# Kernel tuning notes

Measured on AMD Instinct MI355X. Metric: run time of the kernel, lower is better.

The kernel has to match this reference:

```python
import jax, jax.numpy as jnp
import numpy as np

NODE_DIM = 128
N_NODES = 100000
N_EDGES = 600000


def setup_inputs() -> dict:
    key = jax.random.key(0)
    k_x, k_e, k_w1, k_b1, k_w2, k_b2 = jax.random.split(key, 6)
    x = jax.random.normal(k_x, (N_NODES, NODE_DIM), dtype=jnp.float32)
    edge_index = jax.random.randint(k_e, (2, N_EDGES), 0, N_NODES, dtype=jnp.int64)
    # nn.Linear default init: U(-1/sqrt(fan_in), 1/sqrt(fan_in))
    lim1 = 1.0 / np.sqrt(2 * NODE_DIM)
    W1 = jax.random.uniform(k_w1, (2 * NODE_DIM, NODE_DIM), minval=-lim1, maxval=lim1, dtype=jnp.float32)
    b1 = jax.random.uniform(k_b1, (NODE_DIM,), minval=-lim1, maxval=lim1, dtype=jnp.float32)
    lim2 = 1.0 / np.sqrt(NODE_DIM)
    W2 = jax.random.uniform(k_w2, (NODE_DIM, 1), minval=-lim2, maxval=lim2, dtype=jnp.float32)
    b2 = jax.random.uniform(k_b2, (1,), minval=-lim2, maxval=lim2, dtype=jnp.float32)
    return {"x": x, "edge_index": edge_index, "W1": W1, "b1": b1, "W2": W2, "b2": b2}


def reference(x, edge_index, W1, b1, W2, b2):
    src = edge_index[0]
    dst = edge_index[1]
    # [E, 2*node_dim] gathered pair features
    pair = jnp.concatenate([x[src], x[dst]], axis=-1)
    h = jax.nn.relu(pair @ W1 + b1)          # [E, node_dim]
    s = jax.nn.sigmoid(h @ W2 + b2)          # [E, 1]
    return s.squeeze(-1)                      # [E]
```

## Files before the change

kernel.cpp:

```cpp
#include <hip/hip_runtime.h>
#include <hip/hip_bf16.h>
#include <stdint.h>

#define NODE_DIM 128
#define N_NODES  100000
#define N_EDGES  600000
#define NOUT     256

#define QSTEP_INV 64.0f
#define QSTEP     (1.0f / 64.0f)

typedef __bf16 bf16x8 __attribute__((ext_vector_type(8)));
typedef float  f32x4  __attribute__((ext_vector_type(4)));

static __device__ inline unsigned pack2_bf16(float a, float b) {
    unsigned short ua = __builtin_bit_cast(unsigned short, (__bf16)a);
    unsigned short ub = __builtin_bit_cast(unsigned short, (__bf16)b);
    return (unsigned)ua | ((unsigned)ub << 16);
}

static __device__ __forceinline__ void async_copy16(const float* g, void* l) {
    __builtin_amdgcn_global_load_lds(
        (__attribute__((address_space(1))) void*)(uintptr_t)g,
        (__attribute__((address_space(3))) void*)(uint32_t)(uintptr_t)l,
        16, 0, 0);
}

__global__ void wprep_kernel(const float* __restrict__ W1, __bf16* __restrict__ Wt) {
    int i = blockIdx.x * 256 + threadIdx.x;
    if (i >= NOUT * NODE_DIM) return;
    int kp = i >> 7;
    int n  = i & 127;
    float v = W1[i];
    int np = (kp < NODE_DIM) ? n  : (n + NODE_DIM);
    int k  = (kp < NODE_DIM) ? kp : (kp - NODE_DIM);
    Wt[np * NODE_DIM + k] = (__bf16)v;
}

#define MT   64
#define ELD  264

__global__ __launch_bounds__(256)
void gemm_pre_kernel(const float* __restrict__ x, const __bf16* __restrict__ Wt,
                     const float* __restrict__ b1,
                     unsigned char* __restrict__ Ai, unsigned char* __restrict__ Bi) {
    __shared__ __align__(16) char lds_raw[MT * ELD * 2];
    const float* Xf = (const float*)lds_raw;
    __bf16 (*Ls)[ELD] = (__bf16 (*)[ELD])lds_raw;

    const int t    = threadIdx.x;
    const int wave = t >> 6;
    const int lane = t & 63;
    const int lm   = lane & 15;
    const int q    = lane >> 4;
    const int m0   = blockIdx.x * MT;
    const int n0   = wave * 64;

#pragma unroll
    for (int i = 0; i < 8; ++i) {
        const int sbase = i * 256 + wave * 64;
        const int s  = sbase + lane;
        const int R  = s >> 5;
        const int p  = s & 31;
        const int cg = p ^ (R & 7);
        int gr = m0 + R;
        if (gr > N_NODES - 1) gr = N_NODES - 1;
        async_copy16(x + (size_t)gr * NODE_DIM + cg * 4, lds_raw + (size_t)sbase * 16);
    }

    bf16x8 bfr[4][4];
#pragma unroll
    for (int nt = 0; nt < 4; ++nt) {
        const int n = n0 + nt * 16 + lm;
#pragma unroll
        for (int ks = 0; ks < 4; ++ks)
            bfr[nt][ks] = __builtin_bit_cast(bf16x8,
                *(const uint4*)(Wt + (size_t)n * NODE_DIM + ks * 32 + q * 8));
    }

    __syncthreads();

    f32x4 acc[4][4];
#pragma unroll
    for (int a = 0; a < 4; ++a)
#pragma unroll
        for (int b = 0; b < 4; ++b)
            acc[a][b] = (f32x4){0.f, 0.f, 0.f, 0.f};

#pragma unroll
    for (int mt = 0; mt < 4; ++mt) {
        const int R  = mt * 16 + lm;
        const int rs = R & 7;
#pragma unroll
        for (int ks = 0; ks < 4; ++ks) {
            const int c0 = ks * 8 + q * 2;
            const float4 f0 = *(const float4*)&Xf[(R * 32 + (c0 ^ rs)) * 4];
            const float4 f1 = *(const float4*)&Xf[(R * 32 + ((c0 + 1) ^ rs)) * 4];
            uint4 p;
            p.x = pack2_bf16(f0.x, f0.y);
            p.y = pack2_bf16(f0.z, f0.w);
            p.z = pack2_bf16(f1.x, f1.y);
            p.w = pack2_bf16(f1.z, f1.w);
            bf16x8 af = __builtin_bit_cast(bf16x8, p);
#pragma unroll
            for (int nt = 0; nt < 4; ++nt)
                acc[mt][nt] = __builtin_amdgcn_mfma_f32_16x16x32_bf16(
                    af, bfr[nt][ks], acc[mt][nt], 0, 0, 0);
        }
    }

    __syncthreads();

#pragma unroll
    for (int nt = 0; nt < 4; ++nt) {
        const int n = n0 + nt * 16 + lm;
        const float bias = (n < NODE_DIM) ? b1[n] : 0.f;
#pragma unroll
        for (int mt = 0; mt < 4; ++mt) {
#pragma unroll
            for (int r = 0; r < 4; ++r)
                Ls[mt * 16 + q * 4 + r][n] = (__bf16)(acc[mt][nt][r] + bias);
        }
    }
    __syncthreads();

    const int grp = t >> 4;
    const int sub = t & 15;
#pragma unroll
    for (int pass = 0; pass < 8; ++pass) {
        const int hr   = pass * 16 + grp;
        const int row  = hr >> 1;
        const int half = hr & 1;
        const uint4 v = *(const uint4*)(&Ls[row][half * 128 + sub * 8]);
        const unsigned* vu = (const unsigned*)&v;
        unsigned u[8];
#pragma unroll
        for (int i = 0; i < 4; ++i) {
            const float fa = __builtin_bit_cast(float, vu[i] << 16);
            const float fb = __builtin_bit_cast(float, vu[i] & 0xffff0000u);
            float ga = fmaf(fa, QSTEP_INV, 128.5f);
            float gb = fmaf(fb, QSTEP_INV, 128.5f);
            ga = fminf(fmaxf(ga, 0.f), 255.f);
            gb = fminf(fmaxf(gb, 0.f), 255.f);
            u[2 * i]     = (unsigned)ga;
            u[2 * i + 1] = (unsigned)gb;
        }
        uint2 pk;
        pk.x = u[0] | (u[1] << 8) | (u[2] << 16) | (u[3] << 24);
        pk.y = u[4] | (u[5] << 8) | (u[6] << 16) | (u[7] << 24);
        const int m = m0 + row;
        if (m < N_NODES)
            *(uint2*)((half ? Bi : Ai) + (size_t)m * NODE_DIM + sub * 8) = pk;
    }
}

__global__ __launch_bounds__(256)
void edge_score_kernel(const unsigned char* __restrict__ Ai,
                       const unsigned char* __restrict__ Bi,
                       const int* __restrict__ idx,
                       const float* __restrict__ W2, const float* __restrict__ b2,
                       float* __restrict__ out) {
    const int t      = threadIdx.x;
    const int sub    = t & 15;
    const int g0     = (blockIdx.x * 256 + t) >> 4;
    const int stride = (gridDim.x * 256) >> 4;

    float w[8];
#pragma unroll
    for (int j = 0; j < 8; ++j) w[j] = W2[sub * 8 + j];
    const float bias2 = b2[0];

    for (int e = g0; e < N_EDGES; e += 2 * stride) {
        const int e1  = e + stride;
        const bool h1 = e1 < N_EDGES;
        const int s0 = idx[e];
        const int d0 = idx[N_EDGES + e];
        const int s1 = h1 ? idx[e1] : s0;
        const int d1 = h1 ? idx[N_EDGES + e1] : d0;

        const uint2 a0 = *(const uint2*)(Ai + (size_t)s0 * NODE_DIM + sub * 8);
        const uint2 b0 = *(const uint2*)(Bi + (size_t)d0 * NODE_DIM + sub * 8);
        const uint2 a1 = *(const uint2*)(Ai + (size_t)s1 * NODE_DIM + sub * 8);
        const uint2 b1v= *(const uint2*)(Bi + (size_t)d1 * NODE_DIM + sub * 8);

        const unsigned aw0[2] = {a0.x, a0.y}, bw0[2] = {b0.x, b0.y};
        const unsigned aw1[2] = {a1.x, a1.y}, bw1[2] = {b1v.x, b1v.y};
        float p0 = 0.f, p1 = 0.f;
#pragma unroll
        for (int wd = 0; wd < 2; ++wd) {
#pragma unroll
            for (int k = 0; k < 4; ++k) {
                const int ua0 = (int)((aw0[wd] >> (8 * k)) & 0xffu);
                const int ub0 = (int)((bw0[wd] >> (8 * k)) & 0xffu);
                const int ua1 = (int)((aw1[wd] >> (8 * k)) & 0xffu);
                const int ub1 = (int)((bw1[wd] >> (8 * k)) & 0xffu);
                const int r0 = max(ua0 + ub0, 256) - 256;
                const int r1 = max(ua1 + ub1, 256) - 256;
                p0 = fmaf((float)r0, w[wd * 4 + k], p0);
                p1 = fmaf((float)r1, w[wd * 4 + k], p1);
            }
        }
        p0 += __shfl_xor(p0, 1);  p1 += __shfl_xor(p1, 1);
        p0 += __shfl_xor(p0, 2);  p1 += __shfl_xor(p1, 2);
        p0 += __shfl_xor(p0, 4);  p1 += __shfl_xor(p1, 4);
        p0 += __shfl_xor(p0, 8);  p1 += __shfl_xor(p1, 8);
        if (sub == 0) {
            out[e] = 1.f / (1.f + __expf(-fmaf(p0, QSTEP, bias2)));
            if (h1) out[e1] = 1.f / (1.f + __expf(-fmaf(p1, QSTEP, bias2)));
        }
    }
}

__global__ __launch_bounds__(128)
void naive_edge_kernel(const float* __restrict__ x, const int* __restrict__ idx,
                       const float* __restrict__ W1, const float* __restrict__ b1,
                       const float* __restrict__ W2, const float* __restrict__ b2,
                       float* __restrict__ out) {
    __shared__ float pair[2 * NODE_DIM];
    __shared__ float red[2];
    int e = blockIdx.x;
    int t = threadIdx.x;
    int s = idx[e], d = idx[N_EDGES + e];
    pair[t]            = x[(size_t)s * NODE_DIM + t];
    pair[NODE_DIM + t] = x[(size_t)d * NODE_DIM + t];
    __syncthreads();
    float acc = b1[t];
    for (int k = 0; k < 2 * NODE_DIM; ++k)
        acc = fmaf(pair[k], W1[k * NODE_DIM + t], acc);
    float c = fmaxf(acc, 0.f) * W2[t];
#pragma unroll
    for (int m = 1; m < 64; m <<= 1) c += __shfl_xor(c, m);
    if ((t & 63) == 0) red[t >> 6] = c;
    __syncthreads();
    if (t == 0) out[e] = 1.f / (1.f + __expf(-(red[0] + red[1] + b2[0])));
}

extern "C" void kernel_launch(void* const* d_in, const int* in_sizes, int n_in,
                              void* d_out, int out_size, void* d_ws, size_t ws_size,
                              hipStream_t stream) {
    const float* x   = (const float*)d_in[0];
    const int*   idx = (const int*)d_in[1];
    const float* W1  = (const float*)d_in[2];
    const float* b1  = (const float*)d_in[3];
    const float* W2  = (const float*)d_in[4];
    const float* b2  = (const float*)d_in[5];
    float* out = (float*)d_out;

    const size_t tab_bytes = (size_t)N_NODES * NODE_DIM;
    const size_t wt_bytes  = (size_t)NOUT * NODE_DIM * sizeof(__bf16);
    const size_t need = 2 * tab_bytes + wt_bytes;

    if (ws_size >= need) {
        unsigned char* Ai = (unsigned char*)d_ws;
        unsigned char* Bi = Ai + tab_bytes;
        __bf16* Wt = (__bf16*)(Bi + tab_bytes);
        hipLaunchKernelGGL(wprep_kernel, dim3(128), dim3(256), 0, stream, W1, Wt);
        hipLaunchKernelGGL(gemm_pre_kernel, dim3((N_NODES + MT - 1) / MT), dim3(256),
                           0, stream, x, Wt, b1, Ai, Bi);
        hipLaunchKernelGGL(edge_score_kernel, dim3(2048), dim3(256), 0, stream,
                           Ai, Bi, idx, W2, b2, out);
    } else {
        hipLaunchKernelGGL(naive_edge_kernel, dim3(N_EDGES), dim3(128), 0, stream,
                           x, idx, W1, b1, W2, b2, out);
    }
}
```

Measured before the change: 137.7 us.

## Restructure edge scoring: 8 lanes per edge, 4 edges per group, wider loads

```diff
diff --git a/kernel.cpp b/kernel.cpp
--- a/kernel.cpp
+++ b/kernel.cpp
@@ -160,54 +160,62 @@
                        const int* __restrict__ idx,
                        const float* __restrict__ W2, const float* __restrict__ b2,
                        float* __restrict__ out) {
-    const int t      = threadIdx.x;
-    const int sub    = t & 15;
-    const int g0     = (blockIdx.x * 256 + t) >> 4;
-    const int stride = (gridDim.x * 256) >> 4;
-
-    float w[8];
-#pragma unroll
-    for (int j = 0; j < 8; ++j) w[j] = W2[sub * 8 + j];
+    const int t   = threadIdx.x;
+    const int sub = t & 7;
+    const int g   = (blockIdx.x * 256 + t) >> 3;
+    const int e0  = g * 4;
+    if (e0 >= N_EDGES) return;
+
+    float w[16];
+#pragma unroll
+    for (int j = 0; j < 16; ++j) w[j] = W2[sub * 16 + j];
     const float bias2 = b2[0];
 
-    for (int e = g0; e < N_EDGES; e += 2 * stride) {
-        const int e1  = e + stride;
-        const bool h1 = e1 < N_EDGES;
-        const int s0 = idx[e];
-        const int d0 = idx[N_EDGES + e];
-        const int s1 = h1 ? idx[e1] : s0;
-        const int d1 = h1 ? idx[N_EDGES + e1] : d0;
-
-        const uint2 a0 = *(const uint2*)(Ai + (size_t)s0 * NODE_DIM + sub * 8);
-        const uint2 b0 = *(const uint2*)(Bi + (size_t)d0 * NODE_DIM + sub * 8);
-        const uint2 a1 = *(const uint2*)(Ai + (size_t)s1 * NODE_DIM + sub * 8);
-        const uint2 b1v= *(const uint2*)(Bi + (size_t)d1 * NODE_DIM + sub * 8);
-
-        const unsigned aw0[2] = {a0.x, a0.y}, bw0[2] = {b0.x, b0.y};
-        const unsigned aw1[2] = {a1.x, a1.y}, bw1[2] = {b1v.x, b1v.y};
-        float p0 = 0.f, p1 = 0.f;
-#pragma unroll
-        for (int wd = 0; wd < 2; ++wd) {
+    const int4 sv = *(const int4*)(idx + e0);
+    const int4 dv = *(const int4*)(idx + N_EDGES + e0);
+    const int s[4] = {sv.x, sv.y, sv.z, sv.w};
+    const int d[4] = {dv.x, dv.y, dv.z, dv.w};
+
+    uint4 av[4], bv[4];
+#pragma unroll
+    for (int i = 0; i < 4; ++i) {
+        av[i] = *(const uint4*)(Ai + (size_t)s[i] * NODE_DIM + sub * 16);
+        bv[i] = *(const uint4*)(Bi + (size_t)d[i] * NODE_DIM + sub * 16);
+    }
+
+    float p[4];
+#pragma unroll
+    for (int i = 0; i < 4; ++i) {
+        const unsigned aw[4] = {av[i].x, av[i].y, av[i].z, av[i].w};
+        const unsigned bw[4] = {bv[i].x, bv[i].y, bv[i].z, bv[i].w};
+        float acc = 0.f;
+#pragma unroll
+        for (int wd = 0; wd < 4; ++wd) {
 #pragma unroll
             for (int k = 0; k < 4; ++k) {
-                const int ua0 = (int)((aw0[wd] >> (8 * k)) & 0xffu);
-                const int ub0 = (int)((bw0[wd] >> (8 * k)) & 0xffu);
-                const int ua1 = (int)((aw1[wd] >> (8 * k)) & 0xffu);
-                const int ub1 = (int)((bw1[wd] >> (8 * k)) & 0xffu);
-                const int r0 = max(ua0 + ub0, 256) - 256;
-                const int r1 = max(ua1 + ub1, 256) - 256;
-                p0 = fmaf((float)r0, w[wd * 4 + k], p0);
-                p1 = fmaf((float)r1, w[wd * 4 + k], p1);
+                const int ua = (int)((aw[wd] >> (8 * k)) & 0xffu);
+                const int ub = (int)((bw[wd] >> (8 * k)) & 0xffu);
+                const int r  = max(ua + ub, 256) - 256;
+                acc = fmaf((float)r, w[wd * 4 + k], acc);
             }
         }
-        p0 += __shfl_xor(p0, 1);  p1 += __shfl_xor(p1, 1);
-        p0 += __shfl_xor(p0, 2);  p1 += __shfl_xor(p1, 2);
-        p0 += __shfl_xor(p0, 4);  p1 += __shfl_xor(p1, 4);
-        p0 += __shfl_xor(p0, 8);  p1 += __shfl_xor(p1, 8);
-        if (sub == 0) {
-            out[e] = 1.f / (1.f + __expf(-fmaf(p0, QSTEP, bias2)));
-            if (h1) out[e1] = 1.f / (1.f + __expf(-fmaf(p1, QSTEP, bias2)));
-        }
+        p[i] = acc;
+    }
+
+#pragma unroll
+    for (int i = 0; i < 4; ++i) {
+        p[i] += __shfl_xor(p[i], 1);
+        p[i] += __shfl_xor(p[i], 2);
+        p[i] += __shfl_xor(p[i], 4);
+    }
+
+    if (sub == 0) {
+        float4 o;
+        o.x = 1.f / (1.f + __expf(-fmaf(p[0], QSTEP, bias2)));
+        o.y = 1.f / (1.f + __expf(-fmaf(p[1], QSTEP, bias2)));
+        o.z = 1.f / (1.f + __expf(-fmaf(p[2], QSTEP, bias2)));
+        o.w = 1.f / (1.f + __expf(-fmaf(p[3], QSTEP, bias2)));
+        *(float4*)(out + e0) = o;
     }
 }
 
@@ -257,8 +265,8 @@
         hipLaunchKernelGGL(wprep_kernel, dim3(128), dim3(256), 0, stream, W1, Wt);
         hipLaunchKernelGGL(gemm_pre_kernel, dim3((N_NODES + MT - 1) / MT), dim3(256),
                            0, stream, x, Wt, b1, Ai, Bi);
-        hipLaunchKernelGGL(edge_score_kernel, dim3(2048), dim3(256), 0, stream,
-                           Ai, Bi, idx, W2, b2, out);
+        hipLaunchKernelGGL(edge_score_kernel, dim3((N_EDGES / 4 + 31) / 32), dim3(256),
+                           0, stream, Ai, Bi, idx, W2, b2, out);
     } else {
         hipLaunchKernelGGL(naive_edge_kernel, dim3(N_EDGES), dim3(128), 0, stream,
                            x, idx, W1, b1, W2, b2, out);
```

After: 132.9 us. -3.5%, faster.
